# Kernel optimization log

Hardware: AMD Instinct MI355X
Metric: run time of the kernel (lower is better)

## Reference

```python
import math
import jax, jax.numpy as jnp
import numpy as np

NUM_BUCKETS = 32
MAX_DISTANCE = 128
N_HEADS = 16
D_KV = 64


def _relative_position_bucket(relative_position, num_buckets=NUM_BUCKETS, max_distance=MAX_DISTANCE):
    # bidirectional (encoder) version, faithful to T5Attention._relative_position_bucket
    nb = num_buckets // 2
    rel_buckets = (relative_position > 0).astype(jnp.int32) * nb
    rp = jnp.abs(relative_position)
    max_exact = nb // 2
    is_small = rp < max_exact
    # log-spaced buckets for large distances; clamp arg of log to >=1 to avoid -inf
    rp_large = max_exact + (
        jnp.log(jnp.maximum(rp, 1).astype(jnp.float32) / max_exact)
        / math.log(max_distance / max_exact)
        * (nb - max_exact)
    ).astype(jnp.int32)
    rp_large = jnp.minimum(rp_large, nb - 1)
    return rel_buckets + jnp.where(is_small, rp, rp_large)


def setup_inputs() -> dict:
    key = jax.random.key(0)
    ks = jax.random.split(key, 6)
    B, S, D = 2, 2048, 1024
    scale = 0.02
    return {
        "hidden_states": jax.random.normal(ks[0], (B, S, D), dtype=jnp.float32),
        "Wq": jax.random.normal(ks[1], (D, N_HEADS * D_KV), dtype=jnp.float32) * scale,
        "Wk": jax.random.normal(ks[2], (D, N_HEADS * D_KV), dtype=jnp.float32) * scale,
        "Wv": jax.random.normal(ks[3], (D, N_HEADS * D_KV), dtype=jnp.float32) * scale,
        "Wo": jax.random.normal(ks[4], (N_HEADS * D_KV, D), dtype=jnp.float32) * scale,
        "rel_bias": jax.random.normal(ks[5], (NUM_BUCKETS, N_HEADS), dtype=jnp.float32),
    }


def reference(hidden_states, Wq, Wk, Wv, Wo, rel_bias):
    B, S, D = hidden_states.shape
    H, dk = N_HEADS, D_KV
    q = (hidden_states @ Wq).reshape(B, S, H, dk)
    k = (hidden_states @ Wk).reshape(B, S, H, dk)
    v = (hidden_states @ Wv).reshape(B, S, H, dk)

    pos = jnp.arange(S)
    relative_position = pos[None, :] - pos[:, None]          # [S_q, S_k]
    buckets = _relative_position_bucket(relative_position)    # [S_q, S_k]
    bias = rel_bias[buckets].transpose(2, 0, 1)               # [H, S_q, S_k]

    # T5 attention: NO 1/sqrt(d) scaling
    scores = jnp.einsum('bqhd,bkhd->bhqk', q, k) + bias[None]
    attn = jax.nn.softmax(scores, axis=-1)
    ctx = jnp.einsum('bhqk,bkhd->bqhd', attn, v).reshape(B, S, H * dk)
    return ctx @ Wo
```

## Files before the change

kernel.cpp:

```cpp
#include <hip/hip_runtime.h>
#include <hip/hip_bf16.h>
#include <stdint.h>

#define S_LEN 2048
#define NH 16
#define NB_DELTA (2*S_LEN-1)
#define PST 72
#define LOG2E 1.4426950408889634f

typedef __attribute__((ext_vector_type(8))) __bf16 bf16x8;
typedef __attribute__((ext_vector_type(4))) float f32x4;

__device__ __forceinline__ unsigned short f2bf(float f){
    union { float f; unsigned int u; } v; v.f = f;
    unsigned int u = v.u;
    return (unsigned short)((u + 0x7FFFu + ((u >> 16) & 1u)) >> 16);
}
__device__ __forceinline__ float bf2f(unsigned short u){
    union { unsigned int u; float f; } v; v.u = ((unsigned int)u) << 16;
    return v.f;
}
__device__ __forceinline__ unsigned int pkbf(float a, float b){
    __hip_bfloat162 h = __float22bfloat162_rn(float2{a, b});
    unsigned int u;
    __builtin_memcpy(&u, &h, 4);
    return u;
}
#if __has_builtin(__builtin_amdgcn_exp2f)
__device__ __forceinline__ float fexp2(float x){ return __builtin_amdgcn_exp2f(x); }
#else
__device__ __forceinline__ float fexp2(float x){ return __expf(x * 0.69314718056f); }
#endif

__device__ __forceinline__ void gload16(const void* g, void* l){
    __builtin_amdgcn_global_load_lds(
        (const __attribute__((address_space(1))) void*)(uintptr_t)g,
        (__attribute__((address_space(3))) void*)(uintptr_t)l, 16, 0, 0);
}

__global__ __launch_bounds__(256) void prep_kernel(
    const float* __restrict__ hs, unsigned short* __restrict__ hsb,
    const float* __restrict__ W0, const float* __restrict__ W1,
    const float* __restrict__ W2, const float* __restrict__ W3,
    unsigned short* __restrict__ D0, unsigned short* __restrict__ D1,
    unsigned short* __restrict__ D2, unsigned short* __restrict__ D3,
    const float* __restrict__ rel_bias, float* __restrict__ biasT){
    if (blockIdx.z == 4) {
        int bi = blockIdx.y * 32 + blockIdx.x;
        for (int it = 0; it < 4; it++) {
            int i = bi * 4096 + it * 1024 + threadIdx.x * 4;
            float4 f = *(const float4*)(hs + i);
            ushort4 o;
            o.x = f2bf(f.x); o.y = f2bf(f.y); o.z = f2bf(f.z); o.w = f2bf(f.w);
            *(ushort4*)(hsb + i) = o;
        }
        if (bi < 16) {
            int t = bi * 256 + threadIdx.x;
            if (t < NB_DELTA) {
                int delta = t - (S_LEN - 1);
                int bucket = (delta > 0) ? 16 : 0;
                int a = delta < 0 ? -delta : delta;
                int b;
                if (a < 8) b = a;
                else {
                    int bl = 33 - __builtin_clz(a * a);
                    b = bl < 15 ? bl : 15;
                }
                bucket += b;
                for (int h = 0; h < NH; h++)
                    biasT[h * NB_DELTA + t] = (rel_bias[bucket * NH + h] - 16.f) * LOG2E;
            }
        }
        return;
    }
    const float* src; unsigned short* dst;
    switch (blockIdx.z) {
        case 0: src = W0; dst = D0; break;
        case 1: src = W1; dst = D1; break;
        case 2: src = W2; dst = D2; break;
        default: src = W3; dst = D3; break;
    }
    __shared__ float tile[32][33];
    int bx = blockIdx.x, by = blockIdx.y;
    int tx = threadIdx.x & 31, ty = threadIdx.x >> 5;
    for (int i = 0; i < 4; i++)
        tile[ty + 8*i][tx] = src[(size_t)(by*32 + ty + 8*i) * 1024 + bx*32 + tx];
    __syncthreads();
    for (int i = 0; i < 4; i++)
        dst[(size_t)(bx*32 + ty + 8*i) * 1024 + by*32 + tx] = f2bf(tile[tx][ty + 8*i]);
}

template<int MODE, int BM>
__global__ __launch_bounds__(256) void gemm_bt_kernel(const unsigned short* __restrict__ A,
                                                      const unsigned short* __restrict__ BT,
                                                      float* __restrict__ C0,
                                                      unsigned short* __restrict__ C1,
                                                      unsigned short* __restrict__ Vt,
                                                      int Kdim, int ldc){
    constexpr int IT = BM / 32;
    __shared__ __align__(16) unsigned short As[BM * 64];
    __shared__ __align__(16) unsigned short Bs[128 * 64];
    const int t = threadIdx.x;
    const int wave = t >> 6, lane = t & 63;
    const int quad = lane >> 4, l16 = lane & 15;
    const int wm = (wave >> 1) * (BM / 2), wn = (wave & 1) * 64;
    const size_t row0 = (size_t)blockIdx.y * BM, col0 = (size_t)blockIdx.x * 128;

    const int srow8 = lane >> 3;
    const int gg = (lane & 7) ^ srow8;
    const unsigned short* gA = A  + (row0 + wave * 8 + srow8) * (size_t)Kdim + gg * 8;
    const unsigned short* gB = BT + (col0 + wave * 8 + srow8) * (size_t)Kdim + gg * 8;

    f32x4 acc[IT][4] = {};

    for (int kt = 0; kt < Kdim; kt += 64) {
        for (int p = 0; p < BM / 32; p++)
            gload16(gA + (size_t)(p * 32) * Kdim + kt, &As[(p * 32 + wave * 8) * 64]);
        for (int p = 0; p < 4; p++)
            gload16(gB + (size_t)(p * 32) * Kdim + kt, &Bs[(p * 32 + wave * 8) * 64]);
        __syncthreads();
        bf16x8 a[2][IT], b[2][4];
        for (int ks = 0; ks < 2; ks++) {
            for (int i = 0; i < IT; i++)
                a[ks][i] = *(const bf16x8*)(&As[(wm + i*16 + l16) * 64 + (((ks*4 + quad) ^ (l16 & 7)) * 8)]);
            for (int j = 0; j < 4; j++)
                b[ks][j] = *(const bf16x8*)(&Bs[(wn + j*16 + l16) * 64 + (((ks*4 + quad) ^ (l16 & 7)) * 8)]);
        }
        for (int ks = 0; ks < 2; ks++)
            for (int i = 0; i < IT; i++)
                for (int j = 0; j < 4; j++)
                    acc[i][j] = __builtin_amdgcn_mfma_f32_16x16x32_bf16(a[ks][i], b[ks][j], acc[i][j], 0, 0, 0);
        __syncthreads();
    }
    for (int i = 0; i < IT; i++)
        for (int j = 0; j < 4; j++) {
            size_t r0 = row0 + wm + i*16 + quad*4;
            size_t c  = col0 + wn + j*16 + l16;
            if (MODE == 0) {
                for (int r = 0; r < 4; r++)
                    C0[(r0 + r) * ldc + c] = acc[i][j][r];
            } else if (c < 2048) {
                float qs = (c < 1024) ? LOG2E : 1.0f;
                for (int r = 0; r < 4; r++)
                    C1[(r0 + r) * ldc + c] = f2bf(acc[i][j][r] * qs);
            } else {
                size_t bb = r0 >> 11, s = r0 & 2047;
                ushort4 o;
                o.x = f2bf(acc[i][j][0]); o.y = f2bf(acc[i][j][1]);
                o.z = f2bf(acc[i][j][2]); o.w = f2bf(acc[i][j][3]);
                *(ushort4*)(Vt + ((bb << 10) + (c - 2048)) * 2048 + s) = o;
            }
        }
}

__global__ __launch_bounds__(512, 4) void flash12_kernel(
    const unsigned short* __restrict__ qkv,
    const unsigned short* __restrict__ vt,
    const float* __restrict__ biasT,
    unsigned short* __restrict__ ctxpb,
    float* __restrict__ rsbuf)
{
    const int qt = blockIdx.x, h = blockIdx.y;
    const int b = blockIdx.z >> 1, ck = blockIdx.z & 1;
    const int kt0 = ck << 10;
    const int t = threadIdx.x;
    const int w = t >> 6, lane = t & 63, quad = lane >> 4, l16 = lane & 15;
    const int q0 = qt * 256;

    __shared__ __align__(16) unsigned short Ks[2][64 * 64];
    __shared__ __align__(16) unsigned short Vs[2][64 * 64];
    __shared__ __align__(16) unsigned short Pb[256 * PST];
    __shared__ float bias_b[1280];

    for (int s = 0; s < 4; s++) {
        int g = t + s * 512;
        int r = g >> 3, c = (g & 7) * 8;
        *(int4*)&Pb[r * PST + c] =
            *(const int4*)(qkv + (size_t)(b * S_LEN + q0 + r) * 3072 + h * 64 + c);
    }
    {
        const float* bsrc = biasT + h * NB_DELTA + (kt0 - q0 + 1792);
        for (int u = t; u < 1279; u += 512) bias_b[u] = bsrc[u];
    }
    const int srow8 = lane >> 3;
    const int gg = (lane & 7) ^ srow8;
    const int swz = (l16 & 7) * 8;
    const unsigned short* kbase = qkv + (size_t)(b * S_LEN + w * 8 + srow8) * 3072 + 1024 + h * 64 + gg * 8;
    const unsigned short* vbase = vt + (size_t)(b * 1024 + h * 64 + w * 8 + srow8) * 2048 + gg * 8;
    gload16(kbase + (size_t)kt0 * 3072, &Ks[0][(w * 8) * 64]);
    gload16(vbase + kt0,                &Vs[0][(w * 8) * 64]);
    __syncthreads();

    bf16x8 qb[2][2];
    for (int nt = 0; nt < 2; nt++)
        for (int ks = 0; ks < 2; ks++)
            qb[ks][nt] = *(const bf16x8*)&Pb[(w * 32 + nt * 16 + l16) * PST + ks * 32 + quad * 8];

    bf16x8 onesA = {};
    if (l16 == 0) {
        const __bf16 one = (__bf16)1.0f;
        for (int e = 0; e < 8; e++) onesA[e] = one;
    }

    f32x4 ctx[4][2] = {};
    f32x4 rsacc[2] = {};
    const int ib0 = 255 + quad * 4 - w * 32 - l16;

    int cur = 0;
    for (int i = 0; i < 16; i++) {
        if (i < 15) {
            int ktn = kt0 + (i + 1) * 64;
            gload16(kbase + (size_t)ktn * 3072, &Ks[cur ^ 1][(w * 8) * 64]);
            gload16(vbase + ktn,                &Vs[cur ^ 1][(w * 8) * 64]);
        }
        f32x4 st[4][2];
        const int ibt = ib0 + i * 64;
        for (int nt = 0; nt < 2; nt++)
            for (int nb = 0; nb < 4; nb++) {
                const float* bp = &bias_b[ibt - nt * 16 + nb * 16];
                st[nb][nt][0] = bp[0]; st[nb][nt][1] = bp[1];
                st[nb][nt][2] = bp[2]; st[nb][nt][3] = bp[3];
            }
        __builtin_amdgcn_s_setprio(1);
        for (int ks = 0; ks < 2; ks++)
            for (int nb = 0; nb < 4; nb++) {
                bf16x8 ka = *(const bf16x8*)&Ks[cur][(nb * 16 + l16) * 64 + (((ks * 4 + quad) * 8) ^ swz)];
                st[nb][0] = __builtin_amdgcn_mfma_f32_16x16x32_bf16(ka, qb[ks][0], st[nb][0], 0, 0, 0);
                st[nb][1] = __builtin_amdgcn_mfma_f32_16x16x32_bf16(ka, qb[ks][1], st[nb][1], 0, 0, 0);
            }
        __builtin_amdgcn_s_setprio(0);
        for (int nt = 0; nt < 2; nt++) {
            for (int nb = 0; nb < 4; nb++) {
                float e0 = fexp2(st[nb][nt][0]);
                float e1 = fexp2(st[nb][nt][1]);
                float e2 = fexp2(st[nb][nt][2]);
                float e3 = fexp2(st[nb][nt][3]);
                uint2 pk; pk.x = pkbf(e0, e1); pk.y = pkbf(e2, e3);
                *(uint2*)&Pb[(w * 32 + nt * 16 + l16) * PST + nb * 16 + quad * 4] = pk;
            }
        }
        __builtin_amdgcn_s_setprio(1);
        for (int ks = 0; ks < 2; ks++) {
            bf16x8 pb0 = *(const bf16x8*)&Pb[(w * 32 + l16) * PST + ks * 32 + quad * 8];
            bf16x8 pb1 = *(const bf16x8*)&Pb[(w * 32 + 16 + l16) * PST + ks * 32 + quad * 8];
            rsacc[0] = __builtin_amdgcn_mfma_f32_16x16x32_bf16(onesA, pb0, rsacc[0], 0, 0, 0);
            rsacc[1] = __builtin_amdgcn_mfma_f32_16x16x32_bf16(onesA, pb1, rsacc[1], 0, 0, 0);
            for (int nd = 0; nd < 4; nd++) {
                bf16x8 va = *(const bf16x8*)&Vs[cur][(nd * 16 + l16) * 64 + (((ks * 4 + quad) * 8) ^ swz)];
                ctx[nd][0] = __builtin_amdgcn_mfma_f32_16x16x32_bf16(va, pb0, ctx[nd][0], 0, 0, 0);
                ctx[nd][1] = __builtin_amdgcn_mfma_f32_16x16x32_bf16(va, pb1, ctx[nd][1], 0, 0, 0);
            }
        }
        __builtin_amdgcn_s_setprio(0);
        __syncthreads();
        cur ^= 1;
    }
    unsigned short* cp = ctxpb + (size_t)ck * 4096 * 1024;
    for (int nt = 0; nt < 2; nt++) {
        int row = b * S_LEN + q0 + w * 32 + nt * 16 + l16;
        if (quad == 0) rsbuf[((size_t)ck * 4096 + row) * 16 + h] = rsacc[nt][0];
        for (int nd = 0; nd < 4; nd++) {
            uint2 pk;
            pk.x = pkbf(ctx[nd][nt][0], ctx[nd][nt][1]);
            pk.y = pkbf(ctx[nd][nt][2], ctx[nd][nt][3]);
            *(uint2*)&cp[(size_t)row * 1024 + h * 64 + nd * 16 + quad * 4] = pk;
        }
    }
}

__global__ __launch_bounds__(256) void combine_kernel(const unsigned short* __restrict__ ctxpb,
                                                      const float* __restrict__ rsbuf,
                                                      unsigned short* __restrict__ ctxb){
    int e = blockIdx.x * 256 + threadIdx.x;
    int row = e >> 8;
    int c4 = (e & 255) * 4;
    int h = c4 >> 6;
    float l = rsbuf[(size_t)row * 16 + h] + rsbuf[((size_t)4096 + row) * 16 + h];
    ushort4 a  = *(const ushort4*)&ctxpb[(size_t)row * 1024 + c4];
    ushort4 b2 = *(const ushort4*)&ctxpb[(size_t)4096 * 1024 + (size_t)row * 1024 + c4];
    float inv = 1.f / l;
    uint2 o;
    o.x = pkbf((bf2f(a.x) + bf2f(b2.x)) * inv, (bf2f(a.y) + bf2f(b2.y)) * inv);
    o.y = pkbf((bf2f(a.z) + bf2f(b2.z)) * inv, (bf2f(a.w) + bf2f(b2.w)) * inv);
    *(uint2*)&ctxb[(size_t)row * 1024 + c4] = o;
}

extern "C" void kernel_launch(void* const* d_in, const int* in_sizes, int n_in,
                              void* d_out, int out_size, void* d_ws, size_t ws_size,
                              hipStream_t stream) {
    const float* hs       = (const float*)d_in[0];
    const float* Wq       = (const float*)d_in[1];
    const float* Wk       = (const float*)d_in[2];
    const float* Wv       = (const float*)d_in[3];
    const float* Wo       = (const float*)d_in[4];
    const float* rel_bias = (const float*)d_in[5];
    float* out = (float*)d_out;

    char* ws = (char*)d_ws;
    float* biasT          = (float*)ws;           ws += 262144;
    unsigned short* hsb   = (unsigned short*)ws;  ws += 8388608;
    unsigned short* WT    = (unsigned short*)ws;  ws += 6291456;
    unsigned short* WoT   = (unsigned short*)ws;  ws += 2097152;
    unsigned short* qkvb  = (unsigned short*)ws;  ws += 25165824;
    unsigned short* Vtg   = (unsigned short*)ws;  ws += 8388608;
    unsigned short* ctxb  = (unsigned short*)ws;  ws += 8388608;
    unsigned short* ctxpb = (unsigned short*)ws;  ws += 16777216;
    float* rsbuf          = (float*)ws;

    prep_kernel<<<dim3(32, 32, 5), 256, 0, stream>>>(
        hs, hsb, Wq, Wk, Wv, Wo,
        WT, WT + 1024 * 1024, WT + 2 * 1024 * 1024, WoT, rel_bias, biasT);

    gemm_bt_kernel<1, 128><<<dim3(24, 32), 256, 0, stream>>>(hsb, WT, nullptr, qkvb, Vtg, 1024, 3072);
    flash12_kernel<<<dim3(S_LEN / 256, NH, 4), 512, 0, stream>>>(qkvb, Vtg, biasT, ctxpb, rsbuf);
    combine_kernel<<<4096, 256, 0, stream>>>(ctxpb, rsbuf, ctxb);
    gemm_bt_kernel<0, 64><<<dim3(8, 64), 256, 0, stream>>>(ctxb, WoT, out, nullptr, nullptr, 1024, 1024);
}
```

Before: 200.1 us.

## Keep softmax P in registers via permlane swaps instead of LDS round-trip

The flash kernel no longer stages the exponentiated score tile P through shared memory. It rearranges the packed bf16 values across lanes with permlane32/permlane16 swaps so they arrive in the MFMA B-operand layout. Q fragments now load straight from global memory into registers, which removes the 36KB Pb buffer and frees LDS for occupancy. Separately, the QKV GEMM switches from 128-row to 64-row tiles with twice the grid. The main risk is the correctness of the permlane layout mapping, and extra VALU work in exchange for less LDS traffic.

```diff
diff --git a/kernel.cpp b/kernel.cpp
--- a/kernel.cpp
+++ b/kernel.cpp
@@ -5,7 +5,6 @@
 #define S_LEN 2048
 #define NH 16
 #define NB_DELTA (2*S_LEN-1)
-#define PST 72
 #define LOG2E 1.4426950408889634f
 
 typedef __attribute__((ext_vector_type(8))) __bf16 bf16x8;
@@ -153,7 +152,7 @@
         }
 }
 
-__global__ __launch_bounds__(512, 4) void flash12_kernel(
+__global__ __launch_bounds__(512, 4) void flash13_kernel(
     const unsigned short* __restrict__ qkv,
     const unsigned short* __restrict__ vt,
     const float* __restrict__ biasT,
@@ -169,15 +168,8 @@
 
     __shared__ __align__(16) unsigned short Ks[2][64 * 64];
     __shared__ __align__(16) unsigned short Vs[2][64 * 64];
-    __shared__ __align__(16) unsigned short Pb[256 * PST];
     __shared__ float bias_b[1280];
 
-    for (int s = 0; s < 4; s++) {
-        int g = t + s * 512;
-        int r = g >> 3, c = (g & 7) * 8;
-        *(int4*)&Pb[r * PST + c] =
-            *(const int4*)(qkv + (size_t)(b * S_LEN + q0 + r) * 3072 + h * 64 + c);
-    }
     {
         const float* bsrc = biasT + h * NB_DELTA + (kt0 - q0 + 1792);
         for (int u = t; u < 1279; u += 512) bias_b[u] = bsrc[u];
@@ -189,12 +181,16 @@
     const unsigned short* vbase = vt + (size_t)(b * 1024 + h * 64 + w * 8 + srow8) * 2048 + gg * 8;
     gload16(kbase + (size_t)kt0 * 3072, &Ks[0][(w * 8) * 64]);
     gload16(vbase + kt0,                &Vs[0][(w * 8) * 64]);
+
+    bf16x8 qb[2][2];
+    {
+        const unsigned short* qbase =
+            qkv + (size_t)(b * S_LEN + q0 + w * 32 + l16) * 3072 + h * 64 + quad * 8;
+        for (int nt = 0; nt < 2; nt++)
+            for (int ks = 0; ks < 2; ks++)
+                qb[ks][nt] = *(const bf16x8*)(qbase + (size_t)nt * 16 * 3072 + ks * 32);
+    }
     __syncthreads();
-
-    bf16x8 qb[2][2];
-    for (int nt = 0; nt < 2; nt++)
-        for (int ks = 0; ks < 2; ks++)
-            qb[ks][nt] = *(const bf16x8*)&Pb[(w * 32 + nt * 16 + l16) * PST + ks * 32 + quad * 8];
 
     bf16x8 onesA = {};
     if (l16 == 0) {
@@ -229,26 +225,34 @@
                 st[nb][1] = __builtin_amdgcn_mfma_f32_16x16x32_bf16(ka, qb[ks][1], st[nb][1], 0, 0, 0);
             }
         __builtin_amdgcn_s_setprio(0);
-        for (int nt = 0; nt < 2; nt++) {
+        uint2 pk[2][4];
+        for (int nt = 0; nt < 2; nt++)
             for (int nb = 0; nb < 4; nb++) {
                 float e0 = fexp2(st[nb][nt][0]);
                 float e1 = fexp2(st[nb][nt][1]);
                 float e2 = fexp2(st[nb][nt][2]);
                 float e3 = fexp2(st[nb][nt][3]);
-                uint2 pk; pk.x = pkbf(e0, e1); pk.y = pkbf(e2, e3);
-                *(uint2*)&Pb[(w * 32 + nt * 16 + l16) * PST + nb * 16 + quad * 4] = pk;
-            }
-        }
+                pk[nt][nb].x = pkbf(e0, e1);
+                pk[nt][nb].y = pkbf(e2, e3);
+            }
         __builtin_amdgcn_s_setprio(1);
         for (int ks = 0; ks < 2; ks++) {
-            bf16x8 pb0 = *(const bf16x8*)&Pb[(w * 32 + l16) * PST + ks * 32 + quad * 8];
-            bf16x8 pb1 = *(const bf16x8*)&Pb[(w * 32 + 16 + l16) * PST + ks * 32 + quad * 8];
-            rsacc[0] = __builtin_amdgcn_mfma_f32_16x16x32_bf16(onesA, pb0, rsacc[0], 0, 0, 0);
-            rsacc[1] = __builtin_amdgcn_mfma_f32_16x16x32_bf16(onesA, pb1, rsacc[1], 0, 0, 0);
+            bf16x8 pbf[2];
+            for (int nt = 0; nt < 2; nt++) {
+                uint2 x0 = pk[nt][2 * ks], x1 = pk[nt][2 * ks + 1];
+                auto sA = __builtin_amdgcn_permlane32_swap(x0.x, x1.x, false, false);
+                auto sB = __builtin_amdgcn_permlane16_swap(sA[0], sA[1], false, false);
+                auto sC = __builtin_amdgcn_permlane32_swap(x0.y, x1.y, false, false);
+                auto sD = __builtin_amdgcn_permlane16_swap(sC[0], sC[1], false, false);
+                unsigned int u4[4] = {sB[0], sD[0], sB[1], sD[1]};
+                __builtin_memcpy(&pbf[nt], u4, 16);
+            }
+            rsacc[0] = __builtin_amdgcn_mfma_f32_16x16x32_bf16(onesA, pbf[0], rsacc[0], 0, 0, 0);
+            rsacc[1] = __builtin_amdgcn_mfma_f32_16x16x32_bf16(onesA, pbf[1], rsacc[1], 0, 0, 0);
             for (int nd = 0; nd < 4; nd++) {
                 bf16x8 va = *(const bf16x8*)&Vs[cur][(nd * 16 + l16) * 64 + (((ks * 4 + quad) * 8) ^ swz)];
-                ctx[nd][0] = __builtin_amdgcn_mfma_f32_16x16x32_bf16(va, pb0, ctx[nd][0], 0, 0, 0);
-                ctx[nd][1] = __builtin_amdgcn_mfma_f32_16x16x32_bf16(va, pb1, ctx[nd][1], 0, 0, 0);
+                ctx[nd][0] = __builtin_amdgcn_mfma_f32_16x16x32_bf16(va, pbf[0], ctx[nd][0], 0, 0, 0);
+                ctx[nd][1] = __builtin_amdgcn_mfma_f32_16x16x32_bf16(va, pbf[1], ctx[nd][1], 0, 0, 0);
             }
         }
         __builtin_amdgcn_s_setprio(0);
@@ -260,10 +264,10 @@
         int row = b * S_LEN + q0 + w * 32 + nt * 16 + l16;
         if (quad == 0) rsbuf[((size_t)ck * 4096 + row) * 16 + h] = rsacc[nt][0];
         for (int nd = 0; nd < 4; nd++) {
-            uint2 pk;
-            pk.x = pkbf(ctx[nd][nt][0], ctx[nd][nt][1]);
-            pk.y = pkbf(ctx[nd][nt][2], ctx[nd][nt][3]);
-            *(uint2*)&cp[(size_t)row * 1024 + h * 64 + nd * 16 + quad * 4] = pk;
+            uint2 pk2;
+            pk2.x = pkbf(ctx[nd][nt][0], ctx[nd][nt][1]);
+            pk2.y = pkbf(ctx[nd][nt][2], ctx[nd][nt][3]);
+            *(uint2*)&cp[(size_t)row * 1024 + h * 64 + nd * 16 + quad * 4] = pk2;
         }
     }
 }
@@ -311,8 +315,8 @@
         hs, hsb, Wq, Wk, Wv, Wo,
         WT, WT + 1024 * 1024, WT + 2 * 1024 * 1024, WoT, rel_bias, biasT);
 
-    gemm_bt_kernel<1, 128><<<dim3(24, 32), 256, 0, stream>>>(hsb, WT, nullptr, qkvb, Vtg, 1024, 3072);
-    flash12_kernel<<<dim3(S_LEN / 256, NH, 4), 512, 0, stream>>>(qkvb, Vtg, biasT, ctxpb, rsbuf);
+    gemm_bt_kernel<1, 64><<<dim3(24, 64), 256, 0, stream>>>(hsb, WT, nullptr, qkvb, Vtg, 1024, 3072);
+    flash13_kernel<<<dim3(S_LEN / 256, NH, 4), 512, 0, stream>>>(qkvb, Vtg, biasT, ctxpb, rsbuf);
     combine_kernel<<<4096, 256, 0, stream>>>(ctxpb, rsbuf, ctxb);
     gemm_bt_kernel<0, 64><<<dim3(8, 64), 256, 0, stream>>>(ctxb, WoT, out, nullptr, nullptr, 1024, 1024);
 }
```

Measured after the change: 190.8 us. 4.7% less time.
